# Optimization experiments

Measured on AMD Instinct MI355X. Metric: run time of the kernel, lower is better.

## Reference

```python
import jax, jax.numpy as jnp
import numpy as np
import math

B, N, K, C = 2, 8192, 16, 64
PE_DIM, HID = 32, 16
SIGMA, EPS = 1.0, 1e-06


def setup_inputs() -> dict:
    key = jax.random.key(0)
    ks = jax.random.split(key, 8)
    p = jax.random.normal(ks[0], (B, N, 3), jnp.float32)
    f = jax.random.normal(ks[1], (B, C, N), jnp.float32)
    pe = jax.random.normal(ks[2], (B, C, N, K), jnp.float32)
    knn_idx = jax.random.randint(ks[3], (B, N, K), 0, N, jnp.int32)
    # LocalAggregation convs1: 1x1 conv [C -> C] (+ReLU)
    W1 = jax.random.normal(ks[4], (C, C), jnp.float32) * (1.0 / math.sqrt(C))
    b1 = jnp.zeros((C,), jnp.float32)
    # GaussianKDEOffsetGenerator params: pe_mlp Linear(3->32), ffn Linear(32->16)->Linear(16->3)
    Wpe = jax.random.normal(ks[5], (PE_DIM, 3), jnp.float32) * (1.0 / math.sqrt(3))
    bpe = jnp.zeros((PE_DIM,), jnp.float32)
    Wh1 = jax.random.normal(ks[6], (HID, PE_DIM), jnp.float32) * (1.0 / math.sqrt(PE_DIM))
    bh1 = jnp.zeros((HID,), jnp.float32)
    Wh2 = jax.random.normal(ks[7], (3, HID), jnp.float32) * (1.0 / math.sqrt(HID))
    bh2 = jnp.zeros((3,), jnp.float32)
    return {"p": p, "f": f, "pe": pe, "W1": W1, "b1": b1, "Wpe": Wpe,
            "bpe": bpe, "Wh1": Wh1, "bh1": bh1, "Wh2": Wh2, "bh2": bh2,
            "knn_idx": knn_idx}


def reference(p, f, pe, W1, b1, Wpe, bpe, Wh1, bh1, Wh2, bh2, knn_idx):
    gather = jax.vmap(lambda a, i: a[i])  # per-batch neighbor gather
    # --- LocalAggregation: convs1 (1x1 conv + relu), group_by_idx, pe+fj, max-pool over K ---
    h = jax.nn.relu(jnp.einsum('oc,bcn->bon', W1, f) + b1[None, :, None])  # [B,C,N]
    ht = jnp.transpose(h, (0, 2, 1))                                       # [B,N,C]
    fj = gather(ht, knn_idx)                                               # [B,N,K,C]
    fout = jnp.max(pe + jnp.transpose(fj, (0, 3, 1, 2)), axis=-1)          # [B,C,N]
    # --- GaussianKDEOffsetGenerator on grouped neighbor coords [B*N, K, 3] ---
    coords = gather(p, knn_idx).reshape(B * N, K, 3)
    rel = coords[:, :, None, :] - coords[:, None, :, :]                    # [BN,K,K,3]
    pek = jax.nn.relu(jnp.einsum('nijc,dc->nijd', rel, Wpe) + bpe).mean(axis=2)  # [BN,K,PE]
    dist2 = jnp.sum(rel * rel, axis=-1)                                    # [BN,K,K]
    coef = 1.0 / math.sqrt(2.0 * math.pi * SIGMA ** 2 + EPS)
    kde = (coef * jnp.exp(-dist2 / (2.0 * SIGMA ** 2 + EPS))).sum(axis=2, keepdims=True)
    kde = kde / (jnp.max(kde, axis=1, keepdims=True) + EPS)                # [BN,K,1]
    fused = pek * kde
    delta = jax.nn.relu(fused @ Wh1.T + bh1) @ Wh2.T + bh2                 # [BN,K,3]
    return (fout, delta)
```

## Files before the change

kernel.cpp:

```cpp
#include <hip/hip_runtime.h>

#define B_ 2
#define N_ 8192
#define K_ 16
#define C_ 64
#define PE_ 32
#define HID_ 16

typedef float f4 __attribute__((ext_vector_type(4)));

__device__ __forceinline__ f4 splat4(float x) { f4 r = {x, x, x, x}; return r; }
__device__ __forceinline__ f4 relu4(f4 v) {
  f4 r;
  r[0] = fmaxf(v[0], 0.f); r[1] = fmaxf(v[1], 0.f);
  r[2] = fmaxf(v[2], 0.f); r[3] = fmaxf(v[3], 0.f);
  return r;
}
__device__ __forceinline__ float dot4(float4 w, f4 v) {
  return fmaf(w.x, v[0], fmaf(w.y, v[1], fmaf(w.z, v[2], w.w * v[3])));
}

struct PK4 { f4 k0, k1, k2, k3; };

__device__ __forceinline__ PK4 channel(const float4* __restrict__ sq,
                                       int d, const float* __restrict__ Wpe,
                                       const float* __restrict__ bpe) {
  const float wx = Wpe[d * 3 + 0], wy = Wpe[d * 3 + 1], wz = Wpe[d * 3 + 2];
  const float wb = bpe[d];
  const float4 A0 = sq[0], B0 = sq[1], C0 = sq[2];
  const float4 A1 = sq[3], B1 = sq[4], C1 = sq[5];
  const float4 A2 = sq[6], B2 = sq[7], C2 = sq[8];
  const float4 A3 = sq[9], B3 = sq[10], C3 = sq[11];
  const float p0  = fmaf(wx, A0.x, fmaf(wy, A0.y, wz * A0.z));
  const float p1  = fmaf(wx, A0.w, fmaf(wy, B0.x, wz * B0.y));
  const float p2  = fmaf(wx, B0.z, fmaf(wy, B0.w, wz * C0.x));
  const float p3  = fmaf(wx, C0.y, fmaf(wy, C0.z, wz * C0.w));
  const float p4  = fmaf(wx, A1.x, fmaf(wy, A1.y, wz * A1.z));
  const float p5  = fmaf(wx, A1.w, fmaf(wy, B1.x, wz * B1.y));
  const float p6  = fmaf(wx, B1.z, fmaf(wy, B1.w, wz * C1.x));
  const float p7  = fmaf(wx, C1.y, fmaf(wy, C1.z, wz * C1.w));
  const float p8  = fmaf(wx, A2.x, fmaf(wy, A2.y, wz * A2.z));
  const float p9  = fmaf(wx, A2.w, fmaf(wy, B2.x, wz * B2.y));
  const float p10 = fmaf(wx, B2.z, fmaf(wy, B2.w, wz * C2.x));
  const float p11 = fmaf(wx, C2.y, fmaf(wy, C2.z, wz * C2.w));
  const float p12 = fmaf(wx, A3.x, fmaf(wy, A3.y, wz * A3.z));
  const float p13 = fmaf(wx, A3.w, fmaf(wy, B3.x, wz * B3.y));
  const float p14 = fmaf(wx, B3.z, fmaf(wy, B3.w, wz * C3.x));
  const float p15 = fmaf(wx, C3.y, fmaf(wy, C3.z, wz * C3.w));
  const f4 a0 = {p0 + wb, p1 + wb, p2 + wb, p3 + wb};
  const f4 a1 = {p4 + wb, p5 + wb, p6 + wb, p7 + wb};
  const f4 a2 = {p8 + wb, p9 + wb, p10 + wb, p11 + wb};
  const f4 a3 = {p12 + wb, p13 + wb, p14 + wb, p15 + wb};
  f4 k0 = splat4(0.f), k1 = splat4(0.f), k2 = splat4(0.f), k3 = splat4(0.f);
#define KSTEP(PJ)                                  \
  {                                                \
    const f4 sp = splat4(PJ);                      \
    k0 += relu4(a0 - sp); k1 += relu4(a1 - sp);    \
    k2 += relu4(a2 - sp); k3 += relu4(a3 - sp);    \
  }
  KSTEP(p0) KSTEP(p1) KSTEP(p2) KSTEP(p3) KSTEP(p4) KSTEP(p5) KSTEP(p6)
  KSTEP(p7) KSTEP(p8) KSTEP(p9) KSTEP(p10) KSTEP(p11) KSTEP(p12) KSTEP(p13)
  KSTEP(p14) KSTEP(p15)
#undef KSTEP
  PK4 r; r.k0 = k0; r.k1 = k1; r.k2 = k2; r.k3 = k3;
  return r;
}

__global__ __launch_bounds__(256) void k1v3(
    const float* __restrict__ f, const float* __restrict__ W1,
    const float* __restrict__ b1, float* __restrict__ ht) {
  __shared__ float sf[C_ * 20];
  const int t = threadIdx.x;
  const int g0 = blockIdx.x * 16;
  const int b = g0 >> 13;
  const int n0 = g0 & (N_ - 1);
  {
    const int c = t >> 2, off = (t & 3) * 4;
    const f4 v = *reinterpret_cast<const f4*>(f + (size_t)(b * C_ + c) * N_ + n0 + off);
    *reinterpret_cast<f4*>(&sf[c * 20 + off]) = v;
  }
  __syncthreads();
  const int lane = t & 63;
  const int w = t >> 6;
  const f4* wp = reinterpret_cast<const f4*>(W1 + lane * C_);
  const f4 w0 = wp[0], w1 = wp[1], w2 = wp[2], w3 = wp[3];
  const f4 w4 = wp[4], w5 = wp[5], w6 = wp[6], w7 = wp[7];
  const f4 w8 = wp[8], w9 = wp[9], w10 = wp[10], w11 = wp[11];
  const f4 w12 = wp[12], w13 = wp[13], w14 = wp[14], w15 = wp[15];
  f4 a = splat4(0.f);
#define CSTEP(Q, E)                                                         \
  {                                                                         \
    const f4 fv = *reinterpret_cast<const f4*>(&sf[(Q * 4 + E) * 20 + w * 4]); \
    a += splat4(w##Q[E]) * fv;                                              \
  }
#define CQ(Q) CSTEP(Q, 0) CSTEP(Q, 1) CSTEP(Q, 2) CSTEP(Q, 3)
  CQ(0) CQ(1) CQ(2) CQ(3) CQ(4) CQ(5) CQ(6) CQ(7)
  CQ(8) CQ(9) CQ(10) CQ(11) CQ(12) CQ(13) CQ(14) CQ(15)
#undef CQ
#undef CSTEP
  const float bias = b1[lane];
  #pragma unroll
  for (int pt = 0; pt < 4; ++pt)
    ht[(size_t)(b * N_ + n0 + w * 4 + pt) * C_ + lane] = fmaxf(a[pt] + bias, 0.f);
}

#define SFJ_STRIDE 65
#define SOUT_OFF 16640
#define NP2 1024
__global__ __launch_bounds__(256) void k23_split(
    const float* __restrict__ p, const float* __restrict__ pe,
    const float* __restrict__ ht, const int* __restrict__ knn,
    const float* __restrict__ Wpe, const float* __restrict__ bpe,
    const float* __restrict__ Wh1, const float* __restrict__ bh1,
    const float* __restrict__ Wh2, const float* __restrict__ bh2,
    float* __restrict__ fout, float* __restrict__ delta) {
  __shared__ __align__(16) char smem[21760];
  const int t = threadIdx.x;

  if (blockIdx.x < NP2) {
    float* sfj = (float*)smem;
    float* sout = (float*)(smem + SOUT_OFF);
    const int base = blockIdx.x * 16;
    const int b = base >> 13;
    const int n0b = base & (N_ - 1);
    const int lane = t & 63;
    const int w = t >> 6;
    const int csub = lane >> 4, sl = lane & 15;
    const int j = sl & 3, nn = sl >> 2;
    #pragma unroll 1
    for (int si = 0; si < 4; ++si) {
      const int n0 = n0b + si * 4;
      #pragma unroll
      for (int n = 0; n < 4; ++n) {
        const int* kn = knn + (size_t)(b * N_ + n0 + n) * K_ + w * 4;
        #pragma unroll
        for (int kk = 0; kk < 4; ++kk) {
          const int id = kn[kk];
          const float hv = ht[(size_t)(b * N_ + id) * C_ + lane];
          sfj[lane * SFJ_STRIDE + (n * 4 + w) * 4 + kk] = hv;
        }
      }
      __syncthreads();
      #pragma unroll
      for (int it2 = 0; it2 < 4; ++it2) {
        const int c = it2 * 16 + w * 4 + csub;
        const f4 pv = __builtin_nontemporal_load(
            reinterpret_cast<const f4*>(pe + ((size_t)(b * C_ + c) * N_ + n0) * K_) + sl);
        const f4 fj = *reinterpret_cast<const f4*>(&sfj[c * SFJ_STRIDE + sl * 4]);
        float v = fmaxf(fmaxf(pv[0] + fj[0], pv[1] + fj[1]),
                        fmaxf(pv[2] + fj[2], pv[3] + fj[3]));
        v = fmaxf(v, __shfl_xor(v, 1));
        v = fmaxf(v, __shfl_xor(v, 2));
        if (j == 0) sout[c * 20 + si * 4 + nn] = v;
      }
      __syncthreads();
    }
    const int c = t >> 2, q = t & 3;
    const float4 r = *reinterpret_cast<const float4*>(&sout[c * 20 + q * 4]);
    *reinterpret_cast<float4*>(fout + (size_t)(b * C_ + c) * N_ + n0b + q * 4) = r;
    return;
  }

  {
    float* spk = (float*)smem;
    float* sc = (float*)(smem + 16384);
    const int base = (blockIdx.x - NP2) * 8;
    const int b = base >> 13;
    const int g = t >> 5;
    const int l = t & 31;

    if (l < 16) {
      const int gid = base + g;
      const int idx = knn[(size_t)gid * K_ + l];
      const float* pp = p + (size_t)(b * N_ + idx) * 3;
      sc[g * 48 + l * 3 + 0] = pp[0];
      sc[g * 48 + l * 3 + 1] = pp[1];
      sc[g * 48 + l * 3 + 2] = pp[2];
    }
    __syncthreads();

    {
      const int d = l;
      const float4* sq = reinterpret_cast<const float4*>(&sc[g * 48]);
      const PK4 ck = channel(sq, d, Wpe, bpe);
      const int qw = d >> 2, pos = d & 3;
      float* gbase = spk + g * 512;
#define PKW(II, KV) \
      gbase[(II) * 32 + (((qw ^ ((II) & 7)) << 2) | pos)] = ck.KV[(II) & 3];
      PKW(0, k0) PKW(1, k0) PKW(2, k0) PKW(3, k0)
      PKW(4, k1) PKW(5, k1) PKW(6, k1) PKW(7, k1)
      PKW(8, k2) PKW(9, k2) PKW(10, k2) PKW(11, k2)
      PKW(12, k3) PKW(13, k3) PKW(14, k3) PKW(15, k3)
#undef PKW
    }
    __syncthreads();

    {
      const int i = t & 15, half = (t >> 4) & 1;
      const int gid = base + g;
      const float ci0 = sc[g * 48 + i * 3 + 0];
      const float ci1 = sc[g * 48 + i * 3 + 1];
      const float ci2 = sc[g * 48 + i * 3 + 2];
      const float4* sq = reinterpret_cast<const float4*>(&sc[g * 48]);
      const float INV2S = 0.49999975f;
      const float COEF = 0.39894225f;
      float kacc = 0.f;
      #pragma unroll
      for (int jj = 0; jj < 2; ++jj) {
        const int j4 = half * 2 + jj;
        const float4 a = sq[j4 * 3 + 0], b4 = sq[j4 * 3 + 1], c4 = sq[j4 * 3 + 2];
        float dx, dy, dz;
        dx = ci0 - a.x;  dy = ci1 - a.y;  dz = ci2 - a.z;
        kacc += __expf(-(dx * dx + dy * dy + dz * dz) * INV2S);
        dx = ci0 - a.w;  dy = ci1 - b4.x; dz = ci2 - b4.y;
        kacc += __expf(-(dx * dx + dy * dy + dz * dz) * INV2S);
        dx = ci0 - b4.z; dy = ci1 - b4.w; dz = ci2 - c4.x;
        kacc += __expf(-(dx * dx + dy * dy + dz * dz) * INV2S);
        dx = ci0 - c4.y; dy = ci1 - c4.z; dz = ci2 - c4.w;
        kacc += __expf(-(dx * dx + dy * dy + dz * dz) * INV2S);
      }
      kacc += __shfl_xor(kacc, 16);
      const float kde = COEF * kacc;
      float m = kde;
      m = fmaxf(m, __shfl_xor(m, 1));
      m = fmaxf(m, __shfl_xor(m, 2));
      m = fmaxf(m, __shfl_xor(m, 4));
      m = fmaxf(m, __shfl_xor(m, 8));
      const float s = (kde / (m + 1e-6f)) * (1.f / 16.f);

      const float* rbase = spk + g * 512 + i * 32;
      const int ix = i & 7;
      const f4 v0 = *reinterpret_cast<const f4*>(&rbase[(0 ^ ix) << 2]);
      const f4 v1 = *reinterpret_cast<const f4*>(&rbase[(1 ^ ix) << 2]);
      const f4 v2 = *reinterpret_cast<const f4*>(&rbase[(2 ^ ix) << 2]);
      const f4 v3 = *reinterpret_cast<const f4*>(&rbase[(3 ^ ix) << 2]);
      const f4 v4 = *reinterpret_cast<const f4*>(&rbase[(4 ^ ix) << 2]);
      const f4 v5 = *reinterpret_cast<const f4*>(&rbase[(5 ^ ix) << 2]);
      const f4 v6 = *reinterpret_cast<const f4*>(&rbase[(6 ^ ix) << 2]);
      const f4 v7 = *reinterpret_cast<const f4*>(&rbase[(7 ^ ix) << 2]);

      float o0 = 0.f, o1 = 0.f, o2 = 0.f;
      #pragma unroll
      for (int hh = 0; hh < 8; ++hh) {
        const int h = half * 8 + hh;
        const float4* Wr = reinterpret_cast<const float4*>(Wh1 + h * PE_);
        const float u = dot4(Wr[0], v0) + dot4(Wr[1], v1) + dot4(Wr[2], v2) +
                        dot4(Wr[3], v3) + dot4(Wr[4], v4) + dot4(Wr[5], v5) +
                        dot4(Wr[6], v6) + dot4(Wr[7], v7);
        const float a = fmaxf(fmaf(s, u, bh1[h]), 0.f);
        o0 = fmaf(Wh2[0 * HID_ + h], a, o0);
        o1 = fmaf(Wh2[1 * HID_ + h], a, o1);
        o2 = fmaf(Wh2[2 * HID_ + h], a, o2);
      }
      o0 += __shfl_xor(o0, 16);
      o1 += __shfl_xor(o1, 16);
      o2 += __shfl_xor(o2, 16);
      if (half == 0) {
        float* dp = delta + ((size_t)gid * K_ + i) * 3;
        dp[0] = o0 + bh2[0];
        dp[1] = o1 + bh2[1];
        dp[2] = o2 + bh2[2];
      }
    }
  }
}

extern "C" void kernel_launch(void* const* d_in, const int* in_sizes, int n_in,
                              void* d_out, int out_size, void* d_ws, size_t ws_size,
                              hipStream_t stream) {
  const float* p   = (const float*)d_in[0];
  const float* f   = (const float*)d_in[1];
  const float* pe  = (const float*)d_in[2];
  const float* W1  = (const float*)d_in[3];
  const float* b1  = (const float*)d_in[4];
  const float* Wpe = (const float*)d_in[5];
  const float* bpe = (const float*)d_in[6];
  const float* Wh1 = (const float*)d_in[7];
  const float* bh1 = (const float*)d_in[8];
  const float* Wh2 = (const float*)d_in[9];
  const float* bh2 = (const float*)d_in[10];
  const int* knn   = (const int*)d_in[11];
  float* fout  = (float*)d_out;
  float* delta = (float*)d_out + (size_t)B_ * C_ * N_;
  float* ht = (float*)d_ws;

  k1v3<<<(B_ * N_) / 16, 256, 0, stream>>>(f, W1, b1, ht);
  k23_split<<<NP2 + (B_ * N_) / 8, 256, 0, stream>>>(
      p, pe, ht, knn, Wpe, bpe, Wh1, bh1, Wh2, bh2, fout, delta);
}
```

Baseline: 60.46 us.

## Software-pipeline neighbor gathers and prefetch all pe tiles into registers

Rewrites the fout path's four-step loop as a manually unrolled pipeline. All sixteen pe vectors are loaded into registers up front, and the gather of the next sub-tile's neighbor features into registers overlaps the max-reduction of the current sub-tile from shared memory. This hides global load latency of the random ht gathers and the pe stream. In exchange it raises register pressure, which could cut occupancy, and it adds an extra barrier per stage.

```diff
diff --git a/kernel.cpp b/kernel.cpp
--- a/kernel.cpp
+++ b/kernel.cpp
@@ -127,34 +127,93 @@
     const int w = t >> 6;
     const int csub = lane >> 4, sl = lane & 15;
     const int j = sl & 3, nn = sl >> 2;
-    #pragma unroll 1
-    for (int si = 0; si < 4; ++si) {
-      const int n0 = n0b + si * 4;
-      #pragma unroll
-      for (int n = 0; n < 4; ++n) {
-        const int* kn = knn + (size_t)(b * N_ + n0 + n) * K_ + w * 4;
-        #pragma unroll
-        for (int kk = 0; kk < 4; ++kk) {
-          const int id = kn[kk];
-          const float hv = ht[(size_t)(b * N_ + id) * C_ + lane];
-          sfj[lane * SFJ_STRIDE + (n * 4 + w) * 4 + kk] = hv;
-        }
-      }
-      __syncthreads();
-      #pragma unroll
-      for (int it2 = 0; it2 < 4; ++it2) {
-        const int c = it2 * 16 + w * 4 + csub;
-        const f4 pv = __builtin_nontemporal_load(
-            reinterpret_cast<const f4*>(pe + ((size_t)(b * C_ + c) * N_ + n0) * K_) + sl);
-        const f4 fj = *reinterpret_cast<const f4*>(&sfj[c * SFJ_STRIDE + sl * 4]);
-        float v = fmaxf(fmaxf(pv[0] + fj[0], pv[1] + fj[1]),
-                        fmaxf(pv[2] + fj[2], pv[3] + fj[3]));
-        v = fmaxf(v, __shfl_xor(v, 1));
-        v = fmaxf(v, __shfl_xor(v, 2));
-        if (j == 0) sout[c * 20 + si * 4 + nn] = v;
-      }
-      __syncthreads();
-    }
+
+#define PV(SI, IT2)                                                            \
+    const f4 pv_##SI##_##IT2 = __builtin_nontemporal_load(                     \
+        reinterpret_cast<const f4*>(                                           \
+            pe + ((size_t)(b * C_ + (IT2) * 16 + w * 4 + csub) * N_ +          \
+                  n0b + (SI) * 4) * K_) + sl);
+    PV(0, 0) PV(0, 1) PV(0, 2) PV(0, 3)
+    PV(1, 0) PV(1, 1) PV(1, 2) PV(1, 3)
+    PV(2, 0) PV(2, 1) PV(2, 2) PV(2, 3)
+    PV(3, 0) PV(3, 1) PV(3, 2) PV(3, 3)
+#undef PV
+
+    float g0, g1, g2, g3, g4, g5, g6, g7, g8, g9, g10, g11, g12, g13, g14, g15;
+#define GATHER(SI)                                                             \
+    {                                                                          \
+      const int n0g = n0b + (SI) * 4;                                          \
+      const int* kn0 = knn + (size_t)(b * N_ + n0g + 0) * K_ + w * 4;          \
+      const int* kn1 = knn + (size_t)(b * N_ + n0g + 1) * K_ + w * 4;          \
+      const int* kn2 = knn + (size_t)(b * N_ + n0g + 2) * K_ + w * 4;          \
+      const int* kn3 = knn + (size_t)(b * N_ + n0g + 3) * K_ + w * 4;          \
+      g0  = ht[(size_t)(b * N_ + kn0[0]) * C_ + lane];                         \
+      g1  = ht[(size_t)(b * N_ + kn0[1]) * C_ + lane];                         \
+      g2  = ht[(size_t)(b * N_ + kn0[2]) * C_ + lane];                         \
+      g3  = ht[(size_t)(b * N_ + kn0[3]) * C_ + lane];                         \
+      g4  = ht[(size_t)(b * N_ + kn1[0]) * C_ + lane];                         \
+      g5  = ht[(size_t)(b * N_ + kn1[1]) * C_ + lane];                         \
+      g6  = ht[(size_t)(b * N_ + kn1[2]) * C_ + lane];                         \
+      g7  = ht[(size_t)(b * N_ + kn1[3]) * C_ + lane];                         \
+      g8  = ht[(size_t)(b * N_ + kn2[0]) * C_ + lane];                         \
+      g9  = ht[(size_t)(b * N_ + kn2[1]) * C_ + lane];                         \
+      g10 = ht[(size_t)(b * N_ + kn2[2]) * C_ + lane];                         \
+      g11 = ht[(size_t)(b * N_ + kn2[3]) * C_ + lane];                         \
+      g12 = ht[(size_t)(b * N_ + kn3[0]) * C_ + lane];                         \
+      g13 = ht[(size_t)(b * N_ + kn3[1]) * C_ + lane];                         \
+      g14 = ht[(size_t)(b * N_ + kn3[2]) * C_ + lane];                         \
+      g15 = ht[(size_t)(b * N_ + kn3[3]) * C_ + lane];                         \
+    }
+#define WRITE_SFJ                                                              \
+    {                                                                          \
+      float* rowp = &sfj[lane * SFJ_STRIDE + w * 4];                           \
+      rowp[0 * 16 + 0] = g0;  rowp[0 * 16 + 1] = g1;                           \
+      rowp[0 * 16 + 2] = g2;  rowp[0 * 16 + 3] = g3;                           \
+      rowp[1 * 16 + 0] = g4;  rowp[1 * 16 + 1] = g5;                           \
+      rowp[1 * 16 + 2] = g6;  rowp[1 * 16 + 3] = g7;                           \
+      rowp[2 * 16 + 0] = g8;  rowp[2 * 16 + 1] = g9;                           \
+      rowp[2 * 16 + 2] = g10; rowp[2 * 16 + 3] = g11;                          \
+      rowp[3 * 16 + 0] = g12; rowp[3 * 16 + 1] = g13;                          \
+      rowp[3 * 16 + 2] = g14; rowp[3 * 16 + 3] = g15;                          \
+    }
+#define CONS1(SI, IT2)                                                         \
+    {                                                                          \
+      const int c = (IT2) * 16 + w * 4 + csub;                                 \
+      const f4 fj = *reinterpret_cast<const f4*>(&sfj[c * SFJ_STRIDE + sl * 4]); \
+      float v = fmaxf(fmaxf(pv_##SI##_##IT2[0] + fj[0],                        \
+                            pv_##SI##_##IT2[1] + fj[1]),                       \
+                      fmaxf(pv_##SI##_##IT2[2] + fj[2],                        \
+                            pv_##SI##_##IT2[3] + fj[3]));                      \
+      v = fmaxf(v, __shfl_xor(v, 1));                                          \
+      v = fmaxf(v, __shfl_xor(v, 2));                                          \
+      if (j == 0) sout[c * 20 + (SI) * 4 + nn] = v;                            \
+    }
+#define CONSUME(SI) CONS1(SI, 0) CONS1(SI, 1) CONS1(SI, 2) CONS1(SI, 3)
+
+    GATHER(0)
+    WRITE_SFJ
+    __syncthreads();
+    GATHER(1)
+    CONSUME(0)
+    __syncthreads();
+    WRITE_SFJ
+    __syncthreads();
+    GATHER(2)
+    CONSUME(1)
+    __syncthreads();
+    WRITE_SFJ
+    __syncthreads();
+    GATHER(3)
+    CONSUME(2)
+    __syncthreads();
+    WRITE_SFJ
+    __syncthreads();
+    CONSUME(3)
+    __syncthreads();
+#undef CONSUME
+#undef CONS1
+#undef WRITE_SFJ
+#undef GATHER
     const int c = t >> 2, q = t & 3;
     const float4 r = *reinterpret_cast<const float4*>(&sout[c * 20 + q * 4]);
     *reinterpret_cast<float4*>(fout + (size_t)(b * C_ + c) * N_ + n0b + q * 4) = r;
```

Result: slower. 62.29 us (+3.0%).
